# Optimization experiments

Measured on AMD Instinct MI355X. Metric: run time of the kernel, lower is better.

The kernel has to match this reference:

```python
import jax, jax.numpy as jnp
import numpy as np

N, D = 100000, 32      # rows / columns of dist & angle
H, W = 100000, 32      # rows / columns of index matrices
NUM_CLASSES = 22       # size of the eye() one-hot table


def setup_inputs() -> dict:
    key = jax.random.key(0)
    k1, k2, k3, k4, k5 = jax.random.split(key, 5)
    dist = jax.random.uniform(k1, (N, D), dtype=jnp.float32)
    angle = jax.random.uniform(k2, (N, D), dtype=jnp.float32)
    idx_t = jax.random.randint(k3, (H, W), 0, NUM_CLASSES, dtype=jnp.int32)
    index_t = jax.random.randint(k4, (H, W), 0, D + 1, dtype=jnp.int32)
    index_h = jax.random.randint(k5, (H,), 0, N, dtype=jnp.int32)
    return {"dist": dist, "angle": angle, "idx_t": idx_t,
            "index_t": index_t, "index_h": index_h}


def reference(dist, angle, idx_t, index_t, index_h):
    n = dist.shape[0]
    # append a zero column so index D acts as a padding sentinel
    zcol = jnp.zeros((n, 1), dtype=dist.dtype)
    dist_new = jnp.concatenate([dist, zcol], axis=1)    # [N, D+1]
    angle_new = jnp.concatenate([angle, zcol], axis=1)  # [N, D+1]

    h, w = idx_t.shape
    # torch builds ab = index_h @ ones(1, w); equivalent to a broadcast
    ab = jnp.broadcast_to(index_h[:, None], (h, w))     # [h, w]

    dist_t = dist_new[ab, index_t]    # [h, w] gather
    angle_t = angle_new[ab, index_t]  # [h, w] gather

    # eye(22)[idx_t] one-hot lookup, flattened per row -> [h, 22*w]
    x1 = jax.nn.one_hot(idx_t, NUM_CLASSES, dtype=dist.dtype).reshape(h, -1)

    # global min-max normalize of the gathered distances
    dmin = dist_t.min()
    dmax = dist_t.max()
    dist_n = (dist_t - dmin) / (dmax - dmin)

    # [h, 22*w + w + w]
    return jnp.concatenate([x1, dist_n, angle_t], axis=1)
```

## Files before the change

kernel.cpp:

```cpp
#include <hip/hip_runtime.h>

#define DCOLS 32
#define WCOLS 32
#define NUM_CLASSES 22
#define ONEHOT_COLS (NUM_CLASSES * WCOLS)
#define OUT_COLS (ONEHOT_COLS + WCOLS + WCOLS)

__global__ void init_minmax(int* __restrict__ ws) {
    ws[0] = 0x7f800000;
    ws[1] = 0;
}

__global__ __launch_bounds__(256) void minmax_kernel(
    const float* __restrict__ dist,
    const int*   __restrict__ index_t,
    const int*   __restrict__ index_h,
    int*         __restrict__ ws,
    int total)
{
    float vmin = __int_as_float(0x7f800000);
    float vmax = 0.0f;
    for (int i = blockIdx.x * blockDim.x + threadIdx.x; i < total;
         i += gridDim.x * blockDim.x) {
        const int h  = i >> 5;
        const int it = index_t[i];
        float v = 0.0f;
        if (it < DCOLS) v = dist[index_h[h] * DCOLS + it];
        vmin = fminf(vmin, v);
        vmax = fmaxf(vmax, v);
    }
    #pragma unroll
    for (int off = 32; off > 0; off >>= 1) {
        vmin = fminf(vmin, __shfl_down(vmin, off, 64));
        vmax = fmaxf(vmax, __shfl_down(vmax, off, 64));
    }
    __shared__ float smin[4], smax[4];
    const int lane = threadIdx.x & 63;
    const int wave = threadIdx.x >> 6;
    if (lane == 0) { smin[wave] = vmin; smax[wave] = vmax; }
    __syncthreads();
    if (threadIdx.x == 0) {
        float m = smin[0], M = smax[0];
        #pragma unroll
        for (int k = 1; k < 4; ++k) { m = fminf(m, smin[k]); M = fmaxf(M, smax[k]); }
        atomicMin(ws,     __float_as_int(m));
        atomicMax(ws + 1, __float_as_int(M));
    }
}

__global__ __launch_bounds__(192) void fill_kernel(
    const float* __restrict__ dist,
    const float* __restrict__ angle,
    const int*   __restrict__ idx_t,
    const int*   __restrict__ index_t,
    const int*   __restrict__ index_h,
    const int*   __restrict__ ws,
    float*       __restrict__ out)
{
    const int h   = blockIdx.x;
    const int tid = threadIdx.x;

    __shared__ int   s_idx[WCOLS];
    __shared__ float s_dist[WCOLS];
    __shared__ float s_angle[WCOLS];

    if (tid < WCOLS) {
        const float dmin = __int_as_float(ws[0]);
        const float dmax = __int_as_float(ws[1]);
        const float inv  = 1.0f / (dmax - dmin);
        s_idx[tid] = idx_t[h * WCOLS + tid];
        const int it = index_t[h * WCOLS + tid];
        float dv = 0.0f, av = 0.0f;
        if (it < DCOLS) {
            const int base = index_h[h] * DCOLS;
            dv = dist[base + it];
            av = angle[base + it];
        }
        s_dist[tid]  = (dv - dmin) * inv;
        s_angle[tid] = av;
    }
    __syncthreads();

    const int j0 = tid * 4;
    float vals[4];
    #pragma unroll
    for (int k = 0; k < 4; ++k) {
        const int j = j0 + k;
        float v;
        if (j < ONEHOT_COLS) {
            const int w = j / NUM_CLASSES;
            const int c = j - w * NUM_CLASSES;
            v = (s_idx[w] == c) ? 1.0f : 0.0f;
        } else if (j < ONEHOT_COLS + WCOLS) {
            v = s_dist[j - ONEHOT_COLS];
        } else {
            v = s_angle[j - (ONEHOT_COLS + WCOLS)];
        }
        vals[k] = v;
    }
    float4* o = reinterpret_cast<float4*>(out + (size_t)h * OUT_COLS);
    o[tid] = make_float4(vals[0], vals[1], vals[2], vals[3]);
}

extern "C" void kernel_launch(void* const* d_in, const int* in_sizes, int n_in,
                              void* d_out, int out_size, void* d_ws, size_t ws_size,
                              hipStream_t stream) {
    const float* dist    = (const float*)d_in[0];
    const float* angle   = (const float*)d_in[1];
    const int*   idx_t   = (const int*)d_in[2];
    const int*   index_t = (const int*)d_in[3];
    const int*   index_h = (const int*)d_in[4];
    float*       out     = (float*)d_out;
    int*         ws      = (int*)d_ws;

    const int H     = in_sizes[4];
    const int total = H * WCOLS;

    hipLaunchKernelGGL(init_minmax, dim3(1), dim3(1), 0, stream, ws);
    hipLaunchKernelGGL(minmax_kernel, dim3(2048), dim3(256), 0, stream,
                       dist, index_t, index_h, ws, total);
    hipLaunchKernelGGL(fill_kernel, dim3(H), dim3(192), 0, stream,
                       dist, angle, idx_t, index_t, index_h, ws, out);
}
```

Before: 459.8 us.

## Process four rows per fill block and vectorize the min-max index loads

The fill kernel now handles four output rows per 256-thread block, so it launches a quarter as many blocks, and each thread writes three float4s. The min-max pass reads index_t as int4, grouping four gathers per iteration, and runs with half the grid. The one-thread init kernel is replaced by a memset, paired with a sign-flipped unsigned atomicMin encoding so the all-ones initial value works. The aim is lower launch and block-scheduling overhead and better load efficiency, at the cost of extra tail-handling branches.

New measurement: 408.2 us. -11.2%, faster.

```diff
diff --git a/kernel.cpp b/kernel.cpp
--- a/kernel.cpp
+++ b/kernel.cpp
@@ -5,29 +5,30 @@
 #define NUM_CLASSES 22
 #define ONEHOT_COLS (NUM_CLASSES * WCOLS)
 #define OUT_COLS (ONEHOT_COLS + WCOLS + WCOLS)
+#define ROWS_PER_BLOCK 4
 
-__global__ void init_minmax(int* __restrict__ ws) {
-    ws[0] = 0x7f800000;
-    ws[1] = 0;
-}
 
 __global__ __launch_bounds__(256) void minmax_kernel(
     const float* __restrict__ dist,
     const int*   __restrict__ index_t,
     const int*   __restrict__ index_h,
-    int*         __restrict__ ws,
-    int total)
+    unsigned*    __restrict__ ws,
+    int total4)
 {
     float vmin = __int_as_float(0x7f800000);
     float vmax = 0.0f;
-    for (int i = blockIdx.x * blockDim.x + threadIdx.x; i < total;
-         i += gridDim.x * blockDim.x) {
-        const int h  = i >> 5;
-        const int it = index_t[i];
-        float v = 0.0f;
-        if (it < DCOLS) v = dist[index_h[h] * DCOLS + it];
-        vmin = fminf(vmin, v);
-        vmax = fmaxf(vmax, v);
+    const int stride = gridDim.x * blockDim.x;
+    for (int i4 = blockIdx.x * blockDim.x + threadIdx.x; i4 < total4; i4 += stride) {
+        const int4 it = reinterpret_cast<const int4*>(index_t)[i4];
+        const int  h  = i4 >> 3;
+        const int  row = index_h[h] * DCOLS;
+        float v0 = 0.0f, v1 = 0.0f, v2 = 0.0f, v3 = 0.0f;
+        if (it.x < DCOLS) v0 = dist[row + it.x];
+        if (it.y < DCOLS) v1 = dist[row + it.y];
+        if (it.z < DCOLS) v2 = dist[row + it.z];
+        if (it.w < DCOLS) v3 = dist[row + it.w];
+        vmin = fminf(fminf(fminf(vmin, v0), fminf(v1, v2)), v3);
+        vmax = fmaxf(fmaxf(fmaxf(vmax, v0), fmaxf(v1, v2)), v3);
     }
     #pragma unroll
     for (int off = 32; off > 0; off >>= 1) {
@@ -43,63 +44,81 @@
         float m = smin[0], M = smax[0];
         #pragma unroll
         for (int k = 1; k < 4; ++k) { m = fminf(m, smin[k]); M = fmaxf(M, smax[k]); }
-        atomicMin(ws,     __float_as_int(m));
-        atomicMax(ws + 1, __float_as_int(M));
+        atomicMin(ws,              __float_as_uint(-m));
+        atomicMax((int*)(ws + 1),  __float_as_int(M));
     }
 }
 
-__global__ __launch_bounds__(192) void fill_kernel(
+__global__ __launch_bounds__(256) void fill_kernel(
     const float* __restrict__ dist,
     const float* __restrict__ angle,
     const int*   __restrict__ idx_t,
     const int*   __restrict__ index_t,
     const int*   __restrict__ index_h,
-    const int*   __restrict__ ws,
-    float*       __restrict__ out)
+    const unsigned* __restrict__ ws,
+    float*       __restrict__ out,
+    int H)
 {
-    const int h   = blockIdx.x;
+    const int h0  = blockIdx.x * ROWS_PER_BLOCK;
     const int tid = threadIdx.x;
 
-    __shared__ int   s_idx[WCOLS];
-    __shared__ float s_dist[WCOLS];
-    __shared__ float s_angle[WCOLS];
+    __shared__ int   s_idx[ROWS_PER_BLOCK][WCOLS];
+    __shared__ float s_dist[ROWS_PER_BLOCK][WCOLS];
+    __shared__ float s_angle[ROWS_PER_BLOCK][WCOLS];
 
-    if (tid < WCOLS) {
-        const float dmin = __int_as_float(ws[0]);
-        const float dmax = __int_as_float(ws[1]);
+    if (tid < ROWS_PER_BLOCK * WCOLS) {
+        const float dmin = -__uint_as_float(ws[0]);
+        const float dmax =  __uint_as_float(ws[1]);
         const float inv  = 1.0f / (dmax - dmin);
-        s_idx[tid] = idx_t[h * WCOLS + tid];
-        const int it = index_t[h * WCOLS + tid];
-        float dv = 0.0f, av = 0.0f;
-        if (it < DCOLS) {
-            const int base = index_h[h] * DCOLS;
-            dv = dist[base + it];
-            av = angle[base + it];
+        const int r = tid >> 5;
+        const int c = tid & 31;
+        const int h = h0 + r;
+        if (h < H) {
+            const int it = index_t[h * WCOLS + c];
+            s_idx[r][c] = idx_t[h * WCOLS + c];
+            float dv = 0.0f, av = 0.0f;
+            if (it < DCOLS) {
+                const int base = index_h[h] * DCOLS;
+                dv = dist[base + it];
+                av = angle[base + it];
+            }
+            s_dist[r][c]  = (dv - dmin) * inv;
+            s_angle[r][c] = av;
         }
-        s_dist[tid]  = (dv - dmin) * inv;
-        s_angle[tid] = av;
     }
     __syncthreads();
 
-    const int j0 = tid * 4;
-    float vals[4];
+    const bool full = (h0 + ROWS_PER_BLOCK) <= H;
     #pragma unroll
-    for (int k = 0; k < 4; ++k) {
-        const int j = j0 + k;
-        float v;
-        if (j < ONEHOT_COLS) {
-            const int w = j / NUM_CLASSES;
-            const int c = j - w * NUM_CLASSES;
-            v = (s_idx[w] == c) ? 1.0f : 0.0f;
-        } else if (j < ONEHOT_COLS + WCOLS) {
-            v = s_dist[j - ONEHOT_COLS];
-        } else {
-            v = s_angle[j - (ONEHOT_COLS + WCOLS)];
+    for (int m = 0; m < 3; ++m) {
+        const int t    = m * 256 + tid;
+        const int row  = t / 192;
+        const int col4 = t - row * 192;
+        const int j0   = col4 * 4;
+        float vals[4];
+        #pragma unroll
+        for (int k = 0; k < 4; ++k) {
+            const int j = j0 + k;
+            float v;
+            if (j < ONEHOT_COLS) {
+                const int w = j / NUM_CLASSES;
+                const int c = j - w * NUM_CLASSES;
+                v = (s_idx[row][w] == c) ? 1.0f : 0.0f;
+            } else if (j < ONEHOT_COLS + WCOLS) {
+                v = s_dist[row][j - ONEHOT_COLS];
+            } else {
+                v = s_angle[row][j - (ONEHOT_COLS + WCOLS)];
+            }
+            vals[k] = v;
         }
-        vals[k] = v;
+        if (full) {
+            float4* o = reinterpret_cast<float4*>(out + (size_t)h0 * OUT_COLS);
+            o[t] = make_float4(vals[0], vals[1], vals[2], vals[3]);
+        } else if (h0 + row < H) {
+            float4* o = reinterpret_cast<float4*>(out + (size_t)(h0 + row) * OUT_COLS);
+            o[col4] = make_float4(vals[0], vals[1], vals[2], vals[3]);
+        }
     }
-    float4* o = reinterpret_cast<float4*>(out + (size_t)h * OUT_COLS);
-    o[tid] = make_float4(vals[0], vals[1], vals[2], vals[3]);
 }
 
 extern "C" void kernel_launch(void* const* d_in, const int* in_sizes, int n_in,
@@ -111,14 +130,17 @@
     const int*   index_t = (const int*)d_in[3];
     const int*   index_h = (const int*)d_in[4];
     float*       out     = (float*)d_out;
-    int*         ws      = (int*)d_ws;
+    unsigned*    ws      = (unsigned*)d_ws;
 
-    const int H     = in_sizes[4];
-    const int total = H * WCOLS;
+    const int H      = in_sizes[4];
+    const int total4 = (H * WCOLS) / 4;
 
-    hipLaunchKernelGGL(init_minmax, dim3(1), dim3(1), 0, stream, ws);
-    hipLaunchKernelGGL(minmax_kernel, dim3(2048), dim3(256), 0, stream,
-                       dist, index_t, index_h, ws, total);
-    hipLaunchKernelGGL(fill_kernel, dim3(H), dim3(192), 0, stream,
-                       dist, angle, idx_t, index_t, index_h, ws, out);
+    hipMemsetAsync(ws, 0xFF, 8, stream);
+
+    hipLaunchKernelGGL(minmax_kernel, dim3(1024), dim3(256), 0, stream,
+                       dist, index_t, index_h, ws, total4);
+
+    const int fill_blocks = (H + ROWS_PER_BLOCK - 1) / ROWS_PER_BLOCK;
+    hipLaunchKernelGGL(fill_kernel, dim3(fill_blocks), dim3(256), 0, stream,
+                       dist, angle, idx_t, index_t, index_h, ws, out, H);
 }
```
